# Kernel optimization log

Hardware: AMD Instinct MI355X
Metric: run time of the kernel (lower is better)

## Reference

```python
import jax, jax.numpy as jnp
import numpy as np

N_QUBITS = 6
N_LAYERS = 8
N_CLASSES = 4
BATCH = 262144
DIM = 2 ** N_QUBITS  # 64


def setup_inputs() -> dict:
    key = jax.random.key(0)
    k1, k2, k3, k4 = jax.random.split(key, 4)
    x = jax.random.normal(k1, (BATCH, DIM), dtype=jnp.float32)
    # TorchLayer default init for StronglyEntanglingLayers weights: U(0, 2*pi)
    weights = jax.random.uniform(k2, (N_LAYERS, N_QUBITS, 3), dtype=jnp.float32,
                                 minval=0.0, maxval=2.0 * np.pi)
    fc_w = jax.random.normal(k3, (N_CLASSES, N_QUBITS), dtype=jnp.float32) * 0.3
    fc_b = jax.random.normal(k4, (N_CLASSES,), dtype=jnp.float32) * 0.1
    return {"x": x, "weights": weights, "fc_w": fc_w, "fc_b": fc_b}


def _rot_mats(weights):
    # PennyLane Rot(phi, theta, omega) = RZ(omega) RY(theta) RZ(phi)
    phi, theta, omega = weights[..., 0], weights[..., 1], weights[..., 2]
    c = jnp.cos(theta / 2)
    s = jnp.sin(theta / 2)
    m00 = jnp.exp(-0.5j * (phi + omega)) * c
    m01 = -jnp.exp(0.5j * (phi - omega)) * s
    m10 = jnp.exp(-0.5j * (phi - omega)) * s
    m11 = jnp.exp(0.5j * (phi + omega)) * c
    # [L, n, 2, 2] complex64
    return jnp.stack([jnp.stack([m00, m01], -1), jnp.stack([m10, m11], -1)], -2).astype(jnp.complex64)


def _apply_1q(state, U, q):
    # state: [B, 2, 2, 2, 2, 2, 2]; apply 2x2 gate U on qubit axis q+1
    ax = q + 1
    s = jnp.moveaxis(state, ax, -1)
    s = jnp.einsum('ij,...j->...i', U, s)
    return jnp.moveaxis(s, -1, ax)


def _cnot(state, c, t):
    # flip target qubit t on the control==1 slice of qubit c
    axc = c + 1
    s0 = jax.lax.index_in_dim(state, 0, axis=axc, keepdims=False)
    s1 = jax.lax.index_in_dim(state, 1, axis=axc, keepdims=False)
    t_ax = t + 1 if t < c else t  # target axis after removing control axis
    s1 = jnp.flip(s1, axis=t_ax)
    return jnp.stack([s0, s1], axis=axc)


def _pauli_z_signs():
    # qubit 0 is the most significant bit of the basis-state index
    bits = (jnp.arange(DIM)[:, None] >> jnp.arange(N_QUBITS - 1, -1, -1)[None, :]) & 1
    return (1 - 2 * bits).astype(jnp.float32)  # [DIM, N_QUBITS]


def reference(x, weights, fc_w, fc_b):
    B = x.shape[0]
    # F.normalize(p=2) + AmplitudeEmbedding(normalize=True) -> single L2 normalize
    xn = x / jnp.maximum(jnp.linalg.norm(x, axis=1, keepdims=True), 1e-12)
    state = xn.astype(jnp.complex64).reshape((B,) + (2,) * N_QUBITS)
    U = _rot_mats(weights)  # [L, n, 2, 2]
    for l in range(N_LAYERS):
        for q in range(N_QUBITS):
            state = _apply_1q(state, U[l, q], q)
        r = (l % (N_QUBITS - 1)) + 1  # StronglyEntanglingLayers default ranges
        for q in range(N_QUBITS):
            state = _cnot(state, q, (q + r) % N_QUBITS)
    probs = (state.real ** 2 + state.imag ** 2).reshape(B, DIM)
    expvals = probs @ _pauli_z_signs()  # [B, n] <Z_i>
    return expvals @ fc_w.T + fc_b
```

## Files before the change

kernel.cpp:

```cpp
#include <hip/hip_runtime.h>

#define NQ 6
#define DIM 64
#define NL 8

#define KP   136
#define ROWS 128
#define TPB  4

typedef __attribute__((ext_vector_type(8))) short    short8v;
typedef __attribute__((ext_vector_type(4))) float    floatx4;
typedef __attribute__((ext_vector_type(4))) _Float16 half4v;

__device__ inline short f2bf_rne(float f) {
    unsigned u = __float_as_uint(f);
    u += 0x7FFF + ((u >> 16) & 1);
    return (short)(u >> 16);
}

__global__ __launch_bounds__(64) void qnn_prep(
    const float* __restrict__ wts,
    const float* __restrict__ fc_w,
    void* __restrict__ ws)
{
    __shared__ float gc[48][4];
    const int n   = threadIdx.x;
    const int col = blockIdx.x;

    if (n < 48) {
        float phi = wts[n*3+0], th = wts[n*3+1], om = wts[n*3+2];
        float ch = cosf(0.5f*th), sh = sinf(0.5f*th);
        float p  = 0.5f*(phi+om), m  = 0.5f*(phi-om);
        gc[n][0] = cosf(p)*ch;
        gc[n][1] = sinf(p)*ch;
        gc[n][2] = cosf(m)*sh;
        gc[n][3] = sinf(m)*sh;
    }
    __syncthreads();

    float ar = (n == col) ? 1.0f : 0.0f;
    float ai = 0.0f;

    #pragma unroll
    for (int l = 0; l < NL; ++l) {
        #pragma unroll
        for (int q = 0; q < NQ; ++q) {
            const int g     = l*NQ + q;
            const int shift = 5 - q;
            const int mask  = 1 << shift;
            const int b     = (n >> shift) & 1;
            const float cpch = gc[g][0];
            const float spch = gc[g][1];
            const float cmsh = gc[g][2];
            const float smsh = gc[g][3];
            const float pr = __shfl_xor(ar, mask, 64);
            const float pi = __shfl_xor(ai, mask, 64);
            const float udr = cpch;
            const float udi = b ?  spch : -spch;
            const float uor = b ?  cmsh : -cmsh;
            const float uoi = -smsh;
            const float nr = udr*ar - udi*ai + uor*pr - uoi*pi;
            const float ni = udr*ai + udi*ar + uor*pi + uoi*pr;
            ar = nr; ai = ni;
        }
        const int r = (l % (NQ - 1)) + 1;
        #pragma unroll
        for (int q = 0; q < NQ; ++q) {
            const int t     = (q + r) % NQ;
            const int cmask = 1 << (5 - q);
            const int tmask = 1 << (5 - t);
            const float pr = __shfl_xor(ar, tmask, 64);
            const float pi = __shfl_xor(ai, tmask, 64);
            const bool ctrl = (n & cmask) != 0;
            ar = ctrl ? pr : ar;
            ai = ctrl ? pi : ai;
        }
    }

    unsigned short* Bs = (unsigned short*)ws;
    unsigned short hr = (unsigned short)f2bf_rne(ar);
    float hrf = __uint_as_float((unsigned)hr << 16);
    unsigned short lr = (unsigned short)f2bf_rne(ar - hrf);
    unsigned short hi = (unsigned short)f2bf_rne(ai);
    float hif = __uint_as_float((unsigned)hi << 16);
    unsigned short li = (unsigned short)f2bf_rne(ai - hif);
    Bs[n*KP + col]           = hr;
    Bs[n*KP + 64 + col]      = lr;
    Bs[(64+n)*KP + col]      = hi;
    Bs[(64+n)*KP + 64 + col] = li;

    if (col == 0) {
        const int cp = n & 15;
        const int qd = n >> 4;
        half4v* Mo = (half4v*)((char*)ws + 128*KP*2);
        #pragma unroll
        for (int c2 = 0; c2 < 4; ++c2) {
            half4v h4;
            #pragma unroll
            for (int j = 0; j < 4; ++j) {
                const int i = c2*16 + qd*4 + j;
                float v = 0.f;
                if (cp < 4) {
                    #pragma unroll
                    for (int q = 0; q < NQ; ++q) {
                        const float sgn = 1.0f - 2.0f*(float)((i >> (5-q)) & 1);
                        v = fmaf(sgn, fc_w[cp*NQ + q], v);
                    }
                } else if (cp == 4) {
                    v = 1.0f;
                }
                h4[j] = (_Float16)v;
            }
            Mo[c2*64 + n] = h4;
        }
    }
}

__global__ __launch_bounds__(256, 2) void qnn_main(
    const float* __restrict__ x,
    const float* __restrict__ fc_b,
    const void* __restrict__ wsv,
    float* __restrict__ out)
{
    __shared__ __align__(16) unsigned short Bs[128*KP];

    const int tid  = threadIdx.x;
    const int lane = tid & 63;
    const int w    = tid >> 6;
    const int l15  = lane & 15;
    const int quad = lane >> 4;
    const int nb   = gridDim.x;
    const int rbase = w*32 + l15;

    float4 xr[2][2][2][2];
    {
        const float* xt = x + ((size_t)blockIdx.x*ROWS + rbase)*DIM + quad*8;
        #pragma unroll
        for (int st = 0; st < 2; ++st)
            #pragma unroll
            for (int h = 0; h < 2; ++h) {
                xr[0][st][h][0] = *(const float4*)(xt + st*16*DIM + h*32);
                xr[0][st][h][1] = *(const float4*)(xt + st*16*DIM + h*32 + 4);
            }
    }

    {
        const floatx4* bg = (const floatx4*)wsv;
        floatx4* bl = (floatx4*)Bs;
        #pragma unroll
        for (int i = 0; i < 9; ++i) {
            int idx = tid + i*256;
            if (idx < 128*KP*2/16) bl[idx] = bg[idx];
        }
    }

    const half4v* Mg = (const half4v*)((const char*)wsv + 128*KP*2);
    half4v a2[4];
    #pragma unroll
    for (int c2 = 0; c2 < 4; ++c2) a2[c2] = Mg[c2*64 + lane];

    const float b0 = fc_b[0], b1 = fc_b[1], b2 = fc_b[2], b3 = fc_b[3];

    __syncthreads();

    #pragma unroll
    for (int t = 0; t < TPB; ++t) {
        const int buf = t & 1;

        if (t < TPB - 1) {
            const size_t tile1 = (size_t)(blockIdx.x + (t+1)*nb);
            const float* xt = x + (tile1*ROWS + rbase)*DIM + quad*8;
            #pragma unroll
            for (int st = 0; st < 2; ++st)
                #pragma unroll
                for (int h = 0; h < 2; ++h) {
                    xr[buf^1][st][h][0] = *(const float4*)(xt + st*16*DIM + h*32);
                    xr[buf^1][st][h][1] = *(const float4*)(xt + st*16*DIM + h*32 + 4);
                }
        }

        short8v xf[2][2];
        #pragma unroll
        for (int st = 0; st < 2; ++st)
            #pragma unroll
            for (int h = 0; h < 2; ++h) {
                const float4 u0 = xr[buf][st][h][0];
                const float4 u1 = xr[buf][st][h][1];
                short8v a;
                a[0]=f2bf_rne(u0.x); a[1]=f2bf_rne(u0.y);
                a[2]=f2bf_rne(u0.z); a[3]=f2bf_rne(u0.w);
                a[4]=f2bf_rne(u1.x); a[5]=f2bf_rne(u1.y);
                a[6]=f2bf_rne(u1.z); a[7]=f2bf_rne(u1.w);
                xf[st][h] = a;
            }

        floatx4 acc[2][8];
        #pragma unroll
        for (int st = 0; st < 2; ++st)
            #pragma unroll
            for (int mt = 0; mt < 8; ++mt)
                acc[st][mt] = (floatx4){0.f, 0.f, 0.f, 0.f};

        #pragma unroll
        for (int kk = 0; kk < 4; ++kk) {
            const int h  = kk & 1;
            const int bk = (kk << 5) + quad*8;
            #pragma unroll
            for (int mt = 0; mt < 8; ++mt) {
                const short8v wf = *(const short8v*)&Bs[(mt*16 + l15)*KP + bk];
                acc[0][mt] = __builtin_amdgcn_mfma_f32_16x16x32_bf16(wf, xf[0][h], acc[0][mt], 0, 0, 0);
                acc[1][mt] = __builtin_amdgcn_mfma_f32_16x16x32_bf16(wf, xf[1][h], acc[1][mt], 0, 0, 0);
            }
        }

        const size_t s0 = (size_t)(blockIdx.x + t*nb) * ROWS;
        #pragma unroll
        for (int st = 0; st < 2; ++st) {
            floatx4 d2 = (floatx4){0.f, 0.f, 0.f, 0.f};
            #pragma unroll
            for (int c2 = 0; c2 < 4; ++c2) {
                half4v pb;
                #pragma unroll
                for (int r = 0; r < 4; ++r) {
                    const float re = acc[st][c2][r];
                    const float im = acc[st][c2 + 4][r];
                    pb[r] = (_Float16)fmaf(re, re, im*im);
                }
                d2 = __builtin_amdgcn_mfma_f32_16x16x16f16(a2[c2], pb, d2, 0, 0, 0);
            }
            const float ssv = __shfl_xor(d2[0], 16, 64);
            if (quad == 0) {
                const float inv = 1.0f / ssv;
                float4 o;
                o.x = fmaf(d2[0], inv, b0);
                o.y = fmaf(d2[1], inv, b1);
                o.z = fmaf(d2[2], inv, b2);
                o.w = fmaf(d2[3], inv, b3);
                *(float4*)(out + (s0 + w*32 + st*16 + l15)*4) = o;
            }
        }
    }
}

extern "C" void kernel_launch(void* const* d_in, const int* in_sizes, int n_in,
                              void* d_out, int out_size, void* d_ws, size_t ws_size,
                              hipStream_t stream) {
    const float* x    = (const float*)d_in[0];
    const float* wts  = (const float*)d_in[1];
    const float* fc_w = (const float*)d_in[2];
    const float* fc_b = (const float*)d_in[3];
    float* out = (float*)d_out;

    const int batch = in_sizes[0] / DIM;

    qnn_prep<<<DIM, DIM, 0, stream>>>(wts, fc_w, d_ws);
    qnn_main<<<batch / (ROWS*TPB), 256, 0, stream>>>(x, fc_b, d_ws, out);
}
```

Baseline: 106.5 us.

## Process one tile per block with direct global-to-LDS weight loads

Removes the per-block multi-tile loop with register double-buffering, so each block handles a single 128-row tile and the grid grows fourfold. The B matrix is copied into shared memory with global_load_lds, which skips the trip through registers, and the occupancy hint is raised to 3 blocks per CU. The aim is more concurrent waves to hide memory latency. In exchange, every block now reloads the ~35KB weight tile into LDS, so that setup cost is no longer spread over four tiles.

```diff
diff --git a/kernel.cpp b/kernel.cpp
--- a/kernel.cpp
+++ b/kernel.cpp
@@ -6,7 +6,6 @@
 
 #define KP   136
 #define ROWS 128
-#define TPB  4
 
 typedef __attribute__((ext_vector_type(8))) short    short8v;
 typedef __attribute__((ext_vector_type(4))) float    floatx4;
@@ -116,7 +115,7 @@
     }
 }
 
-__global__ __launch_bounds__(256, 2) void qnn_main(
+__global__ __launch_bounds__(256, 3) void qnn_main(
     const float* __restrict__ x,
     const float* __restrict__ fc_b,
     const void* __restrict__ wsv,
@@ -129,28 +128,67 @@
     const int w    = tid >> 6;
     const int l15  = lane & 15;
     const int quad = lane >> 4;
-    const int nb   = gridDim.x;
     const int rbase = w*32 + l15;
 
-    float4 xr[2][2][2][2];
+    float4 xr[2][2][2];
     {
         const float* xt = x + ((size_t)blockIdx.x*ROWS + rbase)*DIM + quad*8;
         #pragma unroll
         for (int st = 0; st < 2; ++st)
             #pragma unroll
             for (int h = 0; h < 2; ++h) {
-                xr[0][st][h][0] = *(const float4*)(xt + st*16*DIM + h*32);
-                xr[0][st][h][1] = *(const float4*)(xt + st*16*DIM + h*32 + 4);
+                xr[st][h][0] = *(const float4*)(xt + st*16*DIM + h*32);
+                xr[st][h][1] = *(const float4*)(xt + st*16*DIM + h*32 + 4);
             }
     }
 
     {
-        const floatx4* bg = (const floatx4*)wsv;
-        floatx4* bl = (floatx4*)Bs;
+        const char* bg = (const char*)wsv;
         #pragma unroll
         for (int i = 0; i < 9; ++i) {
-            int idx = tid + i*256;
-            if (idx < 128*KP*2/16) bl[idx] = bg[idx];
+            const int idx = i*256 + tid;
+            if (idx < 128*KP*2/16) {
+                __builtin_amdgcn_global_load_lds(
+                    (const __attribute__((address_space(1))) unsigned*)(bg + (size_t)idx*16),
+                    (__attribute__((address_space(3))) unsigned*)((char*)Bs + (i*256 + w*64)*16),
+                    16, 0, 0);
+            }
+        }
+    }
+
+    __syncthreads();
+
+    short8v xf[2][2];
+    #pragma unroll
+    for (int st = 0; st < 2; ++st)
+        #pragma unroll
+        for (int h = 0; h < 2; ++h) {
+            const float4 u0 = xr[st][h][0];
+            const float4 u1 = xr[st][h][1];
+            short8v a;
+            a[0]=f2bf_rne(u0.x); a[1]=f2bf_rne(u0.y);
+            a[2]=f2bf_rne(u0.z); a[3]=f2bf_rne(u0.w);
+            a[4]=f2bf_rne(u1.x); a[5]=f2bf_rne(u1.y);
+            a[6]=f2bf_rne(u1.z); a[7]=f2bf_rne(u1.w);
+            xf[st][h] = a;
+        }
+
+    floatx4 acc[2][8];
+    #pragma unroll
+    for (int st = 0; st < 2; ++st)
+        #pragma unroll
+        for (int mt = 0; mt < 8; ++mt)
+            acc[st][mt] = (floatx4){0.f, 0.f, 0.f, 0.f};
+
+    #pragma unroll
+    for (int kk = 0; kk < 4; ++kk) {
+        const int h  = kk & 1;
+        const int bk = (kk << 5) + quad*8;
+        #pragma unroll
+        for (int mt = 0; mt < 8; ++mt) {
+            const short8v wf = *(const short8v*)&Bs[(mt*16 + l15)*KP + bk];
+            acc[0][mt] = __builtin_amdgcn_mfma_f32_16x16x32_bf16(wf, xf[0][h], acc[0][mt], 0, 0, 0);
+            acc[1][mt] = __builtin_amdgcn_mfma_f32_16x16x32_bf16(wf, xf[1][h], acc[1][mt], 0, 0, 0);
         }
     }
 
@@ -158,86 +196,32 @@
     half4v a2[4];
     #pragma unroll
     for (int c2 = 0; c2 < 4; ++c2) a2[c2] = Mg[c2*64 + lane];
-
     const float b0 = fc_b[0], b1 = fc_b[1], b2 = fc_b[2], b3 = fc_b[3];
 
-    __syncthreads();
-
-    #pragma unroll
-    for (int t = 0; t < TPB; ++t) {
-        const int buf = t & 1;
-
-        if (t < TPB - 1) {
-            const size_t tile1 = (size_t)(blockIdx.x + (t+1)*nb);
-            const float* xt = x + (tile1*ROWS + rbase)*DIM + quad*8;
+    const size_t s0 = (size_t)blockIdx.x * ROWS;
+    #pragma unroll
+    for (int st = 0; st < 2; ++st) {
+        floatx4 d2 = (floatx4){0.f, 0.f, 0.f, 0.f};
+        #pragma unroll
+        for (int c2 = 0; c2 < 4; ++c2) {
+            half4v pb;
             #pragma unroll
-            for (int st = 0; st < 2; ++st)
-                #pragma unroll
-                for (int h = 0; h < 2; ++h) {
-                    xr[buf^1][st][h][0] = *(const float4*)(xt + st*16*DIM + h*32);
-                    xr[buf^1][st][h][1] = *(const float4*)(xt + st*16*DIM + h*32 + 4);
-                }
-        }
-
-        short8v xf[2][2];
-        #pragma unroll
-        for (int st = 0; st < 2; ++st)
-            #pragma unroll
-            for (int h = 0; h < 2; ++h) {
-                const float4 u0 = xr[buf][st][h][0];
-                const float4 u1 = xr[buf][st][h][1];
-                short8v a;
-                a[0]=f2bf_rne(u0.x); a[1]=f2bf_rne(u0.y);
-                a[2]=f2bf_rne(u0.z); a[3]=f2bf_rne(u0.w);
-                a[4]=f2bf_rne(u1.x); a[5]=f2bf_rne(u1.y);
-                a[6]=f2bf_rne(u1.z); a[7]=f2bf_rne(u1.w);
-                xf[st][h] = a;
-            }
-
-        floatx4 acc[2][8];
-        #pragma unroll
-        for (int st = 0; st < 2; ++st)
-            #pragma unroll
-            for (int mt = 0; mt < 8; ++mt)
-                acc[st][mt] = (floatx4){0.f, 0.f, 0.f, 0.f};
-
-        #pragma unroll
-        for (int kk = 0; kk < 4; ++kk) {
-            const int h  = kk & 1;
-            const int bk = (kk << 5) + quad*8;
-            #pragma unroll
-            for (int mt = 0; mt < 8; ++mt) {
-                const short8v wf = *(const short8v*)&Bs[(mt*16 + l15)*KP + bk];
-                acc[0][mt] = __builtin_amdgcn_mfma_f32_16x16x32_bf16(wf, xf[0][h], acc[0][mt], 0, 0, 0);
-                acc[1][mt] = __builtin_amdgcn_mfma_f32_16x16x32_bf16(wf, xf[1][h], acc[1][mt], 0, 0, 0);
-            }
-        }
-
-        const size_t s0 = (size_t)(blockIdx.x + t*nb) * ROWS;
-        #pragma unroll
-        for (int st = 0; st < 2; ++st) {
-            floatx4 d2 = (floatx4){0.f, 0.f, 0.f, 0.f};
-            #pragma unroll
-            for (int c2 = 0; c2 < 4; ++c2) {
-                half4v pb;
-                #pragma unroll
-                for (int r = 0; r < 4; ++r) {
-                    const float re = acc[st][c2][r];
-                    const float im = acc[st][c2 + 4][r];
-                    pb[r] = (_Float16)fmaf(re, re, im*im);
-                }
-                d2 = __builtin_amdgcn_mfma_f32_16x16x16f16(a2[c2], pb, d2, 0, 0, 0);
-            }
-            const float ssv = __shfl_xor(d2[0], 16, 64);
-            if (quad == 0) {
-                const float inv = 1.0f / ssv;
-                float4 o;
-                o.x = fmaf(d2[0], inv, b0);
-                o.y = fmaf(d2[1], inv, b1);
-                o.z = fmaf(d2[2], inv, b2);
-                o.w = fmaf(d2[3], inv, b3);
-                *(float4*)(out + (s0 + w*32 + st*16 + l15)*4) = o;
-            }
+            for (int r = 0; r < 4; ++r) {
+                const float re = acc[st][c2][r];
+                const float im = acc[st][c2 + 4][r];
+                pb[r] = (_Float16)fmaf(re, re, im*im);
+            }
+            d2 = __builtin_amdgcn_mfma_f32_16x16x16f16(a2[c2], pb, d2, 0, 0, 0);
+        }
+        const float ssv = __shfl_xor(d2[0], 16, 64);
+        if (quad == 0) {
+            const float inv = 1.0f / ssv;
+            float4 o;
+            o.x = fmaf(d2[0], inv, b0);
+            o.y = fmaf(d2[1], inv, b1);
+            o.z = fmaf(d2[2], inv, b2);
+            o.w = fmaf(d2[3], inv, b3);
+            *(float4*)(out + (s0 + w*32 + st*16 + l15)*4) = o;
         }
     }
 }
@@ -254,5 +238,5 @@
     const int batch = in_sizes[0] / DIM;
 
     qnn_prep<<<DIM, DIM, 0, stream>>>(wts, fc_w, d_ws);
-    qnn_main<<<batch / (ROWS*TPB), 256, 0, stream>>>(x, fc_b, d_ws, out);
-}
+    qnn_main<<<batch / ROWS, 256, 0, stream>>>(x, fc_b, d_ws, out);
+}
```

New measurement: 107.0 us. Within noise of the previous version (+0.4%).
